# Kernel tuning notes

Hardware: AMD Instinct MI355X
Metric: run time of the kernel (lower is better)

The kernel has to match this reference:

```python
import jax, jax.numpy as jnp
import numpy as np

# Each of the 16 differentiable binary logic ops op_k(a,b) is a polynomial
# c0 + ca*a + cb*b + cab*(a*b). Rows follow the standard difflogic op table
# (op 3 = 'a' pass-through, matching the residual init in the source).
_OP2POLY = np.array([
    [0, 0, 0, 0],    # 0: False
    [0, 0, 0, 1],    # 1: a AND b
    [0, 1, 0, -1],   # 2: a AND NOT b
    [0, 1, 0, 0],    # 3: a
    [0, 0, 1, -1],   # 4: NOT a AND b
    [0, 0, 1, 0],    # 5: b
    [0, 1, 1, -2],   # 6: XOR
    [0, 1, 1, -1],   # 7: OR
    [1, -1, -1, 1],  # 8: NOR
    [1, -1, -1, 2],  # 9: XNOR
    [1, 0, -1, 0],   # 10: NOT b
    [1, 0, -1, 1],   # 11: a OR NOT b
    [1, -1, 0, 0],   # 12: NOT a
    [1, -1, 0, 1],   # 13: NOT a OR b
    [1, 0, 0, -1],   # 14: NAND
    [1, 0, 0, 0],    # 15: True
], dtype=np.float32)

KERNEL_SIZE, STRIDE, PADDING, GROUPS, TREE_DEPTH, TAU = 3, 1, 1, 1, 4, 1.0


def setup_inputs() -> dict:
    key = jax.random.key(0)
    k0, k1, k2, k3, k4 = jax.random.split(key, 5)
    B, Cin, H, W = 16, 64, 64, 64
    OC, N = 128, 2 ** TREE_DEPTH
    x = jax.random.uniform(k0, (B, Cin, H, W), dtype=jnp.float32)
    weights = jax.random.normal(k1, (OC, N - 1, 16), dtype=jnp.float32)
    ci = jax.random.randint(k2, (OC, N), 0, Cin // GROUPS, dtype=jnp.int32)
    px = jax.random.randint(k3, (OC, N), 0, KERNEL_SIZE, dtype=jnp.int32)
    py = jax.random.randint(k4, (OC, N), 0, KERNEL_SIZE, dtype=jnp.int32)
    return {"x": x, "weights": weights, "input_channel_indices": ci,
            "input_pos_x_indices": px, "input_pos_y_indices": py}


def _forward(x, weights, ci, px, py):
    B, Cin, H, W = x.shape
    OC = weights.shape[0]
    N = 2 ** TREE_DEPTH
    # Training-mode weights with straight-through estimator:
    # value = one_hot(argmax), gradient flows through softmax.
    w_soft = jax.nn.softmax(weights / TAU, axis=-1).astype(x.dtype)
    w_hard = jax.nn.one_hot(jnp.argmax(weights, axis=-1), 16, dtype=x.dtype)
    w = w_soft + jax.lax.stop_gradient(w_hard - w_soft)
    # [OC, num_gates, 4] polynomial coefficients over (1, a, b, ab)
    coeffs = jnp.einsum('ogk,kc->ogc', w, jnp.asarray(_OP2POLY, x.dtype))

    xp = jnp.pad(x, ((0, 0), (0, 0), (PADDING, PADDING), (PADDING, PADDING)))
    oh = (H + 2 * PADDING - KERNEL_SIZE) // STRIDE + 1
    ow = (W + 2 * PADDING - KERNEL_SIZE) // STRIDE + 1

    icpg = Cin // GROUPS
    group_of_oc = jnp.arange(OC, dtype=jnp.int32) // (OC // GROUPS)
    chan = group_of_oc[:, None] * icpg + ci                       # [OC, N]
    rows = (jnp.arange(oh, dtype=jnp.int32) * STRIDE)[None, None, :] + py[:, :, None]  # [OC,N,oh]
    cols = (jnp.arange(ow, dtype=jnp.int32) * STRIDE)[None, None, :] + px[:, :, None]  # [OC,N,ow]
    # Irregular per-output gather: [B, OC, N, oh, ow]
    vals = xp[:, chan[:, :, None, None], rows[:, :, :, None], cols[:, :, None, :]]

    # Binary tree of logic gates, level by level (gates stored leaf-level first).
    gate_off = 0
    for _ in range(TREE_DEPTH):
        n = vals.shape[2] // 2
        a, b = vals[:, :, 0::2], vals[:, :, 1::2]
        cc = coeffs[:, gate_off:gate_off + n]                     # [OC, n, 4]
        c0, ca, cb, cab = (cc[None, :, :, i, None, None] for i in range(4))
        vals = c0 + ca * a + cb * b + cab * (a * b)
        gate_off += n
    y = vals[:, :, 0]                                             # [B, OC, oh, ow]

    # 2x2 OR-pool (soft OR = 1 - prod(1 - v)), floor division of spatial dims.
    ph, pw = oh // 2, ow // 2
    y = y[:, :, :ph * 2, :pw * 2].reshape(B, OC, ph, 2, pw, 2)
    return 1.0 - jnp.prod(1.0 - y, axis=(3, 5))


def reference(x, weights, input_channel_indices, input_pos_x_indices, input_pos_y_indices):
    return _forward(x, weights, input_channel_indices, input_pos_x_indices, input_pos_y_indices)
```

## Files before the change

kernel.cpp:

```cpp
#include <hip/hip_runtime.h>

#define BATCH 16
#define CIN   64
#define H_    64
#define W_    64
#define IMG   (H_ * W_)
#define OCH   128
#define NLEAF 16
#define NGATE 15
#define PH    32
#define PW    32

#define C_STRIDE_F4 16
#define DESC_OFF    8192

#define ROWS   6
#define RSTR   66
#define CHSTR  (ROWS * RSTR)
#define XSB    2
#define SMEM_F (XSB + CIN * CHSTR)

typedef float f4v __attribute__((ext_vector_type(4)));

__device__ __constant__ __align__(16) float OP2POLY[16][4] = {
    {0, 0, 0, 0}, {0, 0, 0, 1}, {0, 1, 0, -1}, {0, 1, 0, 0},
    {0, 0, 1, -1}, {0, 0, 1, 0}, {0, 1, 1, -2}, {0, 1, 1, -1},
    {1, -1, -1, 1}, {1, -1, -1, 2}, {1, 0, -1, 0}, {1, 0, -1, 1},
    {1, -1, 0, 0}, {1, -1, 0, 1}, {1, 0, 0, -1}, {1, 0, 0, 0}};

__global__ __launch_bounds__(1024) void prep(
    const float* __restrict__ weights,
    const int* __restrict__ ci,
    const int* __restrict__ px,
    const int* __restrict__ py,
    float* __restrict__ ws)
{
    int t = blockIdx.x * 1024 + threadIdx.x;
    if (t < OCH * NGATE) {
        const float* wp = weights + t * 16;
        int best = 0;
        float bv = wp[0];
#pragma unroll
        for (int k = 1; k < 16; ++k) {
            float v = wp[k];
            if (v > bv) { bv = v; best = k; }
        }
        int oc = t / 15, g = t - oc * 15;
        reinterpret_cast<float4*>(ws)[oc * C_STRIDE_F4 + g] =
            reinterpret_cast<const float4*>(OP2POLY)[best];
    } else if (t < OCH * NGATE + OCH * NLEAF) {
        int t2 = t - OCH * NGATE;
        ((int*)ws)[DESC_OFF + t2] =
            XSB + ci[t2] * CHSTR + py[t2] * RSTR + px[t2] - 1;
    }
}

__global__ __launch_bounds__(1024, 4) void logic_tree_main(
    const float* __restrict__ x,
    const float* __restrict__ ws,
    float* __restrict__ out)
{
    __shared__ float smem[SMEM_F];

    const int blk = blockIdx.x;
    const int xcd = blk & 7;
    const int j   = blk >> 3;
    const int b   = (xcd << 1) | (j >> 4);
    const int strip = j & 15;
    const int r0  = strip << 2;
    const int tid = threadIdx.x;

    const float2* xb2 =
        reinterpret_cast<const float2*>(x + (size_t)b * (CIN * IMG));
#pragma unroll
    for (int i = 0; i < 12; ++i) {
        int f   = tid + i * 1024;
        int ch  = f / 192;
        int rem = f - ch * 192;
        int row = rem >> 5;
        int c2  = rem & 31;
        int gr  = r0 - 1 + row;
        float2 val = make_float2(0.f, 0.f);
        if ((unsigned)gr < (unsigned)H_)
            val = xb2[((ch << 6) | gr) * 32 + c2];
        *reinterpret_cast<float2*>(&smem[XSB + ch * CHSTR + row * RSTR + c2 * 2]) = val;
    }
    if (tid < 770) {
        int idx = (tid < 768) ? (XSB + (tid >> 1) * RSTR + 64 + (tid & 1))
                              : (tid - 768);
        smem[idx] = 0.0f;
    }
    __syncthreads();

    const int wave = tid >> 6;
    const int lane = tid & 63;

#pragma unroll 1
    for (int q = 0; q < 8; ++q) {
        const int oc = __builtin_amdgcn_readfirstlane(wave * 8 + q);
        const float4* C4 = reinterpret_cast<const float4*>(ws) + oc * C_STRIDE_F4;
        const int*    D  = ((const int*)ws) + DESC_OFF + oc * NLEAF;

        f4v v[NLEAF];
#pragma unroll
        for (int n = 0; n < NLEAF; ++n) {
            const int base = D[n] + lane;
            v[n].x = smem[base];
            v[n].y = smem[base + RSTR];
            v[n].z = smem[base + 2 * RSTR];
            v[n].w = smem[base + 3 * RSTR];
        }

        int go = 0;
#pragma unroll
        for (int lev = 8; lev >= 1; lev >>= 1) {
#pragma unroll
            for (int t = 0; t < lev; ++t) {
                const float4 cc = C4[go + t];
                f4v a  = v[2 * t];
                f4v bb = v[2 * t + 1];
                v[t] = cc.x + cc.y * a + cc.z * bb + cc.w * (a * bb);
            }
            go += lev;
        }

        float p0 = (1.0f - v[0].x) * (1.0f - v[0].y);
        float p1 = (1.0f - v[0].z) * (1.0f - v[0].w);
        float q0 = p0 * __shfl_xor(p0, 1, 64);
        float q1 = p1 * __shfl_xor(p1, 1, 64);
        float val = (lane & 1) ? (1.0f - q1) : (1.0f - q0);
        out[(((size_t)b * OCH + oc) * PH + (strip << 1) + (lane & 1)) * PW +
            (lane >> 1)] = val;
    }
}

extern "C" void kernel_launch(void* const* d_in, const int* in_sizes, int n_in,
                              void* d_out, int out_size, void* d_ws, size_t ws_size,
                              hipStream_t stream) {
    const float* x       = (const float*)d_in[0];
    const float* weights = (const float*)d_in[1];
    const int*   ci      = (const int*)d_in[2];
    const int*   px      = (const int*)d_in[3];
    const int*   py      = (const int*)d_in[4];
    float* out = (float*)d_out;
    float* ws  = (float*)d_ws;

    prep<<<4, 1024, 0, stream>>>(weights, ci, px, py, ws);
    logic_tree_main<<<BATCH * 16, 1024, 0, stream>>>(x, ws, out);
}
```

Before: 90.76 us.

## Fuse prep kernel into main kernel, storing op indices and descriptors in LDS

Removes the separate prep launch. Each block now computes the argmax op index per gate and the leaf gather offsets itself, storing them in shared memory as packed bytes and ints. Polynomial coefficients are then looked up from the constant OP2POLY table using op indices read once per wave through readfirstlane. This saves a kernel launch and the dependency between the two kernels, but every one of the 256 blocks redoes the argmax over all 1920 gates (about 120KB of weight reads per block) and uses more LDS.

```diff
diff --git a/kernel.cpp b/kernel.cpp
--- a/kernel.cpp
+++ b/kernel.cpp
@@ -11,14 +11,13 @@
 #define PH    32
 #define PW    32
 
-#define C_STRIDE_F4 16
-#define DESC_OFF    8192
-
 #define ROWS   6
 #define RSTR   66
 #define CHSTR  (ROWS * RSTR)
 #define XSB    2
-#define SMEM_F (XSB + CIN * CHSTR)
+#define OPS_F  25348
+#define DS_F   (OPS_F + OCH * 4)
+#define SMEM_F (DS_F + OCH * NLEAF)
 
 typedef float f4v __attribute__((ext_vector_type(4)));
 
@@ -28,39 +27,21 @@
     {1, -1, -1, 1}, {1, -1, -1, 2}, {1, 0, -1, 0}, {1, 0, -1, 1},
     {1, -1, 0, 0}, {1, -1, 0, 1}, {1, 0, 0, -1}, {1, 0, 0, 0}};
 
-__global__ __launch_bounds__(1024) void prep(
+static __device__ __forceinline__ int rfl_i(int v) {
+    return __builtin_amdgcn_readfirstlane(v);
+}
+
+__global__ __launch_bounds__(1024, 4) void logic_tree_fused(
+    const float* __restrict__ x,
     const float* __restrict__ weights,
     const int* __restrict__ ci,
     const int* __restrict__ px,
     const int* __restrict__ py,
-    float* __restrict__ ws)
-{
-    int t = blockIdx.x * 1024 + threadIdx.x;
-    if (t < OCH * NGATE) {
-        const float* wp = weights + t * 16;
-        int best = 0;
-        float bv = wp[0];
-#pragma unroll
-        for (int k = 1; k < 16; ++k) {
-            float v = wp[k];
-            if (v > bv) { bv = v; best = k; }
-        }
-        int oc = t / 15, g = t - oc * 15;
-        reinterpret_cast<float4*>(ws)[oc * C_STRIDE_F4 + g] =
-            reinterpret_cast<const float4*>(OP2POLY)[best];
-    } else if (t < OCH * NGATE + OCH * NLEAF) {
-        int t2 = t - OCH * NGATE;
-        ((int*)ws)[DESC_OFF + t2] =
-            XSB + ci[t2] * CHSTR + py[t2] * RSTR + px[t2] - 1;
-    }
-}
-
-__global__ __launch_bounds__(1024, 4) void logic_tree_main(
-    const float* __restrict__ x,
-    const float* __restrict__ ws,
     float* __restrict__ out)
 {
     __shared__ float smem[SMEM_F];
+    int* smem_i = (int*)smem;
+    unsigned char* smem_b = (unsigned char*)smem;
 
     const int blk = blockIdx.x;
     const int xcd = blk & 7;
@@ -90,25 +71,56 @@
                               : (tid - 768);
         smem[idx] = 0.0f;
     }
+    for (int t = tid; t < OCH * NGATE; t += 1024) {
+        const float4* wp4 = reinterpret_cast<const float4*>(weights + t * 16);
+        const float4 a0 = wp4[0], a1 = wp4[1], a2 = wp4[2], a3 = wp4[3];
+        const float wv[16] = {a0.x, a0.y, a0.z, a0.w, a1.x, a1.y, a1.z, a1.w,
+                              a2.x, a2.y, a2.z, a2.w, a3.x, a3.y, a3.z, a3.w};
+        int best = 0;
+        float bv = wv[0];
+#pragma unroll
+        for (int k = 1; k < 16; ++k)
+            if (wv[k] > bv) { bv = wv[k]; best = k; }
+        int oc = t / 15, g = t - oc * 15;
+        smem_b[OPS_F * 4 + oc * 16 + g] = (unsigned char)best;
+        if (g == 14) smem_b[OPS_F * 4 + oc * 16 + 15] = 0;
+    }
+    for (int t = tid; t < OCH * NLEAF; t += 1024)
+        smem_i[DS_F + t] = XSB + ci[t] * CHSTR + py[t] * RSTR + px[t] - 1;
     __syncthreads();
 
     const int wave = tid >> 6;
     const int lane = tid & 63;
+    const size_t obase0 =
+        (((size_t)b * OCH) * PH + (strip << 1) + (lane & 1)) * PW + (lane >> 1);
 
 #pragma unroll 1
     for (int q = 0; q < 8; ++q) {
-        const int oc = __builtin_amdgcn_readfirstlane(wave * 8 + q);
-        const float4* C4 = reinterpret_cast<const float4*>(ws) + oc * C_STRIDE_F4;
-        const int*    D  = ((const int*)ws) + DESC_OFF + oc * NLEAF;
+        const int oc = wave * 8 + q;
+
+        const uint4 opsv = *reinterpret_cast<const uint4*>(&smem[OPS_F + oc * 4]);
+        const unsigned ou[4] = {
+            (unsigned)rfl_i((int)opsv.x), (unsigned)rfl_i((int)opsv.y),
+            (unsigned)rfl_i((int)opsv.z), (unsigned)rfl_i((int)opsv.w)};
+
+        int base[NLEAF];
+        const int4* D4 = reinterpret_cast<const int4*>(smem_i + DS_F + oc * NLEAF);
+#pragma unroll
+        for (int m = 0; m < 4; ++m) {
+            const int4 d = D4[m];
+            base[4 * m + 0] = d.x + lane;
+            base[4 * m + 1] = d.y + lane;
+            base[4 * m + 2] = d.z + lane;
+            base[4 * m + 3] = d.w + lane;
+        }
 
         f4v v[NLEAF];
 #pragma unroll
         for (int n = 0; n < NLEAF; ++n) {
-            const int base = D[n] + lane;
-            v[n].x = smem[base];
-            v[n].y = smem[base + RSTR];
-            v[n].z = smem[base + 2 * RSTR];
-            v[n].w = smem[base + 3 * RSTR];
+            v[n].x = smem[base[n]];
+            v[n].y = smem[base[n] + RSTR];
+            v[n].z = smem[base[n] + 2 * RSTR];
+            v[n].w = smem[base[n] + 3 * RSTR];
         }
 
         int go = 0;
@@ -116,7 +128,9 @@
         for (int lev = 8; lev >= 1; lev >>= 1) {
 #pragma unroll
             for (int t = 0; t < lev; ++t) {
-                const float4 cc = C4[go + t];
+                const int g  = go + t;
+                const int op = (int)((ou[g >> 2] >> ((g & 3) * 8)) & 255u);
+                const float4 cc = reinterpret_cast<const float4*>(OP2POLY)[op];
                 f4v a  = v[2 * t];
                 f4v bb = v[2 * t + 1];
                 v[t] = cc.x + cc.y * a + cc.z * bb + cc.w * (a * bb);
@@ -129,8 +143,7 @@
         float q0 = p0 * __shfl_xor(p0, 1, 64);
         float q1 = p1 * __shfl_xor(p1, 1, 64);
         float val = (lane & 1) ? (1.0f - q1) : (1.0f - q0);
-        out[(((size_t)b * OCH + oc) * PH + (strip << 1) + (lane & 1)) * PW +
-            (lane >> 1)] = val;
+        out[obase0 + (size_t)oc * (PH * PW)] = val;
     }
 }
 
@@ -143,8 +156,7 @@
     const int*   px      = (const int*)d_in[3];
     const int*   py      = (const int*)d_in[4];
     float* out = (float*)d_out;
-    float* ws  = (float*)d_ws;
+    (void)d_ws; (void)ws_size;
 
-    prep<<<4, 1024, 0, stream>>>(weights, ci, px, py, ws);
-    logic_tree_main<<<BATCH * 16, 1024, 0, stream>>>(x, ws, out);
+    logic_tree_fused<<<BATCH * 16, 1024, 0, stream>>>(x, weights, ci, px, py, out);
 }
```

New measurement: 91.96 us. No clear change (+1.3%).
